# Kernel tuning notes

Measured on AMD Instinct MI355X. Metric: run time of the kernel, lower is better.

The kernel has to match this reference:

```python
import jax, jax.numpy as jnp
import numpy as np

N, F_IN, H, HEADS = 50000, 128, 128, 4
C = H // HEADS
E = 800000


def layer_norm(x, w, b, eps=1e-5):
    mu = x.mean(-1, keepdims=True)
    var = ((x - mu) ** 2).mean(-1, keepdims=True)
    return (x - mu) * jax.lax.rsqrt(var + eps) * w + b


def gat_conv(x, src, dst, edge_attr, W, att_src, att_dst, W_edge, att_edge, bias):
    """PyG GATConv (concat=True, add_self_loops=True, fill_value='mean', edge_dim=H), eval mode."""
    n = x.shape[0]
    # self-loop edge_attr = mean of incoming edge attrs per node (PyG fill_value='mean')
    ones = jnp.ones((src.shape[0],), dtype=edge_attr.dtype)
    deg = jax.ops.segment_sum(ones, dst, n)
    loop_attr = jax.ops.segment_sum(edge_attr, dst, n) / jnp.maximum(deg, 1.0)[:, None]
    loop = jnp.arange(n, dtype=src.dtype)
    src = jnp.concatenate([src, loop])
    dst = jnp.concatenate([dst, loop])
    ea = jnp.concatenate([edge_attr, loop_attr], axis=0)  # [E+N, H]
    h = (x @ W).reshape(n, HEADS, C)                      # [N, heads, C]
    a_src = (h * att_src).sum(-1)                         # [N, heads]
    a_dst = (h * att_dst).sum(-1)
    e = (ea @ W_edge).reshape(-1, HEADS, C)
    a_edge = (e * att_edge).sum(-1)                       # [E+N, heads]
    alpha = jax.nn.leaky_relu(a_src[src] + a_dst[dst] + a_edge, 0.2)
    # segment softmax over destination neighborhoods
    m = jax.lax.stop_gradient(jax.ops.segment_max(alpha, dst, n))
    alpha = jnp.exp(alpha - m[dst])
    s = jax.ops.segment_sum(alpha, dst, n)
    alpha = alpha / (s[dst] + 1e-16)
    out = jax.ops.segment_sum(alpha[:, :, None] * h[src], dst, n)  # [N, heads, C]
    return out.reshape(n, H) + bias


def setup_inputs() -> dict:
    key = jax.random.key(0)
    ks = iter(jax.random.split(key, 40))
    def lin(k, i, o, s=0.05):
        return jax.random.normal(k, (i, o), jnp.float32) * s
    d = {}
    d["x"] = jax.random.normal(next(ks), (N, F_IN), jnp.float32)
    d["edge_time"] = jax.random.uniform(next(ks), (E,), jnp.float32)
    d["ip_w1"] = lin(next(ks), F_IN, 2 * H); d["ip_b1"] = jnp.zeros((2 * H,), jnp.float32)
    d["ip_ln_w"] = jnp.ones((2 * H,), jnp.float32); d["ip_ln_b"] = jnp.zeros((2 * H,), jnp.float32)
    d["ip_w2"] = lin(next(ks), 2 * H, H); d["ip_b2"] = jnp.zeros((H,), jnp.float32)
    d["pn_w"] = jnp.ones((H,), jnp.float32); d["pn_b"] = jnp.zeros((H,), jnp.float32)
    d["ta_w1"] = lin(next(ks), 1, H); d["ta_b1"] = jnp.zeros((H,), jnp.float32)
    d["ta_ln_w"] = jnp.ones((H,), jnp.float32); d["ta_ln_b"] = jnp.zeros((H,), jnp.float32)
    d["ta_w2"] = lin(next(ks), H, H); d["ta_b2"] = jnp.zeros((H,), jnp.float32)
    for p in ("g1", "g2"):
        d[p + "_w"] = lin(next(ks), H, H)
        d[p + "_att_src"] = jax.random.normal(next(ks), (HEADS, C), jnp.float32) * 0.05
        d[p + "_att_dst"] = jax.random.normal(next(ks), (HEADS, C), jnp.float32) * 0.05
        d[p + "_ew"] = lin(next(ks), H, H)
        d[p + "_att_edge"] = jax.random.normal(next(ks), (HEADS, C), jnp.float32) * 0.05
        d[p + "_b"] = jnp.zeros((H,), jnp.float32)
    d["n1_w"] = jnp.ones((H,), jnp.float32); d["n1_b"] = jnp.zeros((H,), jnp.float32)
    d["n2_w"] = jnp.ones((H,), jnp.float32); d["n2_b"] = jnp.zeros((H,), jnp.float32)
    d["edge_index"] = jax.random.randint(next(ks), (2, E), 0, N, jnp.int32)
    return d


def reference(x, edge_time, ip_w1, ip_b1, ip_ln_w, ip_ln_b, ip_w2, ip_b2, pn_w, pn_b,
              ta_w1, ta_b1, ta_ln_w, ta_ln_b, ta_w2, ta_b2,
              g1_w, g1_att_src, g1_att_dst, g1_ew, g1_att_edge, g1_b,
              g2_w, g2_att_src, g2_att_dst, g2_ew, g2_att_edge, g2_b,
              n1_w, n1_b, n2_w, n2_b, edge_index):
    src, dst = edge_index[0], edge_index[1]
    # input projection: Linear -> ReLU -> LayerNorm -> (Dropout eval) -> Linear
    h = jax.nn.relu(x @ ip_w1 + ip_b1)
    h = layer_norm(h, ip_ln_w, ip_ln_b)
    h = h @ ip_w2 + ip_b2
    h = jnp.clip(jax.nn.relu(layer_norm(h, pn_w, pn_b)), -10.0, 10.0)
    # temporal attention MLP on edge times -> per-edge edge_attr [E, H]
    tw = edge_time[:, None] @ ta_w1 + ta_b1
    tw = jax.nn.relu(layer_norm(tw, ta_ln_w, ta_ln_b))
    tw = jnp.clip(jnp.tanh(tw @ ta_w2 + ta_b2), -3.0, 3.0)
    # GAT layer 1 (single chunk => residual + clamp, mean over 1 chunk is identity)
    g = gat_conv(h, src, dst, tw, g1_w, g1_att_src, g1_att_dst, g1_ew, g1_att_edge, g1_b) + h
    g = jax.nn.elu(layer_norm(jnp.clip(g, -10.0, 10.0), n1_w, n1_b))
    # GAT layer 2
    g2 = gat_conv(g, src, dst, tw, g2_w, g2_att_src, g2_att_dst, g2_ew, g2_att_edge, g2_b) + g
    return jax.nn.elu(layer_norm(jnp.clip(g2, -10.0, 10.0), n2_w, n2_b))
```

## Files before the change

kernel.cpp:

```cpp
#include <hip/hip_runtime.h>

typedef unsigned short u16;
typedef __attribute__((ext_vector_type(8))) short bf8_t;
typedef __attribute__((ext_vector_type(4))) float f4_t;

constexpr int NN   = 50000;
constexpr int NE   = 800000;
constexpr int TBLN = 2048;
constexpr int MB64 = (NN + 63) / 64;
constexpr int FB   = NE / 256;

__device__ __forceinline__ u16 f2b(float f) {
  unsigned u = __float_as_uint(f);
  unsigned r = u + 0x7fffu + ((u >> 16) & 1u);
  return (u16)(r >> 16);
}
__device__ __forceinline__ u16 f2h(float f) {
  _Float16 h = (_Float16)f;
  return __builtin_bit_cast(unsigned short, h);
}
__device__ __forceinline__ float h2f(u16 v) {
  _Float16 h = __builtin_bit_cast(_Float16, v);
  return (float)h;
}
__device__ __forceinline__ unsigned packh(float a, float b) {
  return (unsigned)f2h(a) | ((unsigned)f2h(b) << 16);
}
__device__ __forceinline__ float blo(unsigned u) { return __uint_as_float(u << 16); }
__device__ __forceinline__ float bhi(unsigned u) { return __uint_as_float(u & 0xffff0000u); }
__device__ __forceinline__ float wred64(float v) {
#pragma unroll
  for (int o = 32; o; o >>= 1) v += __shfl_xor(v, o);
  return v;
}
__device__ __forceinline__ bf8_t ldv(const u16* p) { return *(const bf8_t*)p; }
__device__ __forceinline__ f4_t mfma16(bf8_t a, bf8_t b, f4_t c) {
  return __builtin_amdgcn_mfma_f32_16x16x32_bf16(a, b, c, 0, 0, 0);
}

__global__ __launch_bounds__(256) void prep_k(
    const float* __restrict__ ew1, const float* __restrict__ ate1,
    const float* __restrict__ ew2, const float* __restrict__ ate2,
    float* __restrict__ V,
    const float* __restrict__ w1, const float* __restrict__ w2,
    const float* __restrict__ gw1, const float* __restrict__ gw2,
    u16* __restrict__ w1t, u16* __restrict__ w2t,
    u16* __restrict__ g1wt, u16* __restrict__ g2wt,
    const int* __restrict__ dstv, int* __restrict__ deg,
    const float* __restrict__ x, u16* __restrict__ x16) {
  const int bid = blockIdx.x, t = threadIdx.x;
  if (bid == 0) {
#pragma unroll
    for (int rep = 0; rep < 2; ++rep) {
      int idx = t + rep * 256;
      int k = idx >> 2, hd = idx & 3;
      float s1 = 0.f, s2 = 0.f;
      for (int c = 0; c < 32; ++c) {
        s1 += ew1[k * 128 + hd * 32 + c] * ate1[hd * 32 + c];
        s2 += ew2[k * 128 + hd * 32 + c] * ate2[hd * 32 + c];
      }
      V[k * 8 + hd] = s1;
      V[k * 8 + 4 + hd] = s2;
    }
  } else if (bid <= 384) {
    int idx = (bid - 1) * 256 + t;
    if (idx < 32768) {
      int r = idx >> 8, c = idx & 255;
      w1t[c * 128 + r] = f2b(w1[idx]);
    } else if (idx < 65536) {
      int k = idx - 32768;
      int r = k >> 7, c = k & 127;
      w2t[c * 256 + r] = f2b(w2[k]);
    } else if (idx < 81920) {
      int k = idx - 65536;
      int r = k >> 7, c = k & 127;
      g1wt[c * 128 + r] = f2b(gw1[k]);
    } else {
      int k = idx - 81920;
      int r = k >> 7, c = k & 127;
      g2wt[c * 128 + r] = f2b(gw2[k]);
    }
  } else if (bid <= 384 + FB) {
    int e = (bid - 385) * 256 + t;
    if (e < NE) atomicAdd(&deg[dstv[e]], 1);
  } else {
    int idx = (bid - 385 - FB) * 256 + t;
    size_t e8 = (size_t)idx * 8;
    const float4 a = *(const float4*)(x + e8);
    const float4 b = *(const float4*)(x + e8 + 4);
    uint4 o;
    o.x = (unsigned)f2b(a.x) | ((unsigned)f2b(a.y) << 16);
    o.y = (unsigned)f2b(a.z) | ((unsigned)f2b(a.w) << 16);
    o.z = (unsigned)f2b(b.x) | ((unsigned)f2b(b.y) << 16);
    o.w = (unsigned)f2b(b.z) | ((unsigned)f2b(b.w) << 16);
    *(uint4*)(x16 + e8) = o;
  }
}

__global__ __launch_bounds__(128) void build_table(
    const float* __restrict__ taw1, const float* __restrict__ tab1,
    const float* __restrict__ talnw, const float* __restrict__ talnb,
    const float* __restrict__ taw2, const float* __restrict__ tab2,
    const float* __restrict__ V, float* __restrict__ tbl) {
  const int j = threadIdx.x;
  const int wv = j >> 6, ln = j & 63;
  const float t = (float)blockIdx.x / (float)(TBLN - 1);
  __shared__ float part[4];
  __shared__ float ush[128];
  __shared__ float pacc[16];
  float v = t * taw1[j] + tab1[j];
  float s = wred64(v), sq = wred64(v * v);
  if (ln == 0) { part[wv * 2] = s; part[wv * 2 + 1] = sq; }
  __syncthreads();
  float S = part[0] + part[2], SQ = part[1] + part[3];
  float mu = S * (1.f / 128.f);
  float var = SQ * (1.f / 128.f) - mu * mu;
  float rstd = rsqrtf(var + 1e-5f);
  float u = fmaxf((v - mu) * rstd * talnw[j] + talnb[j], 0.f);
  ush[j] = u;
  __syncthreads();
  float acc = 0.f;
  for (int k = 0; k < 128; ++k) acc += ush[k] * taw2[k * 128 + j];
  float w = tanhf(acc + tab2[j]);
  w = fminf(fmaxf(w, -3.f), 3.f);
#pragma unroll
  for (int p = 0; p < 8; ++p) {
    float z = wred64(w * V[j * 8 + p]);
    if (ln == 0) pacc[wv * 8 + p] = z;
  }
  __syncthreads();
  if (j < 8) tbl[blockIdx.x * 8 + j] = pacc[j] + pacc[8 + j];
}

__global__ __launch_bounds__(512) void scan1(const int* __restrict__ deg,
                                             int* __restrict__ indptr,
                                             int* __restrict__ blks) {
  const int t = threadIdx.x;
  const int i = blockIdx.x * 512 + t;
  int v = (i < NN) ? deg[i] : 0;
  const int lane = t & 63, wv = t >> 6;
  int x = v;
#pragma unroll
  for (int o = 1; o < 64; o <<= 1) {
    int y = __shfl_up(x, o);
    if (lane >= o) x += y;
  }
  __shared__ int ws[8];
  if (lane == 63) ws[wv] = x;
  __syncthreads();
  if (t < 8) {
    int y = ws[t];
#pragma unroll
    for (int o = 1; o < 8; o <<= 1) {
      int z = __shfl_up(y, o);
      if (t >= o) y += z;
    }
    ws[t] = y;
  }
  __syncthreads();
  int excl = wv ? ws[wv - 1] : 0;
  x += excl;
  if (i < NN) indptr[i + 1] = x;
  if (t == 511) blks[blockIdx.x] = x;
}
__global__ void scan2(int* __restrict__ blks, int nb) {
  const int t = threadIdx.x;
  int v = (t < nb) ? blks[t] : 0;
  const int lane = t & 63, wv = t >> 6;
  int x = v;
#pragma unroll
  for (int o = 1; o < 64; o <<= 1) {
    int y = __shfl_up(x, o);
    if (lane >= o) x += y;
  }
  __shared__ int ws[2];
  if (lane == 63) ws[wv] = x;
  __syncthreads();
  if (wv == 1) x += ws[0];
  if (t < nb) blks[t] = x - v;
}
__global__ __launch_bounds__(512) void scan3(int* __restrict__ indptr,
                                             const int* __restrict__ blks,
                                             const int* __restrict__ deg,
                                             int* __restrict__ cursor) {
  const int i = blockIdx.x * 512 + threadIdx.x;
  if (i < NN) {
    int v = indptr[i + 1] + blks[blockIdx.x];
    indptr[i + 1] = v;
    cursor[i] = v - deg[i];
  }
  if (i == 0) indptr[0] = 0;
}

__device__ void fill_body(int fb, const int* __restrict__ srcv,
                          const int* __restrict__ dstv,
                          const float* __restrict__ etime,
                          const float* __restrict__ tbl,
                          int* __restrict__ cursor,
                          u16* __restrict__ recs) {
  const int e = fb * 256 + threadIdx.x;
  if (e >= NE) return;
  int d = dstv[e];
  int pos = atomicAdd(&cursor[d], 1);
  float t = etime[e];
  t = fminf(fmaxf(t, 0.f), 1.f);
  float fpos = t * (float)(TBLN - 1);
  int i0 = (int)fpos;
  if (i0 > TBLN - 2) i0 = TBLN - 2;
  float fr = fpos - (float)i0;
  const float4* r = (const float4*)(tbl + i0 * 8);
  float4 a0 = r[0], a1 = r[1], b0 = r[2], b1 = r[3];
  float4 o1, o2;
  o1.x = a0.x + fr * (b0.x - a0.x); o1.y = a0.y + fr * (b0.y - a0.y);
  o1.z = a0.z + fr * (b0.z - a0.z); o1.w = a0.w + fr * (b0.w - a0.w);
  o2.x = a1.x + fr * (b1.x - a1.x); o2.y = a1.y + fr * (b1.y - a1.y);
  o2.z = a1.z + fr * (b1.z - a1.z); o2.w = a1.w + fr * (b1.w - a1.w);
  u16* rp = recs + (size_t)pos * 16;
  uint4 w;
  w.x = (unsigned)srcv[e];
  w.y = packh(o1.x, o1.y);
  w.z = packh(o1.z, o1.w);
  w.w = packh(o2.x, o2.y);
  *(uint4*)rp = w;
  *(unsigned*)(rp + 8) = packh(o2.z, o2.w);
}

__device__ void ip_body(int ipb, char* smem,
                        const u16* __restrict__ x16, const u16* __restrict__ w1t,
                        const float* __restrict__ b1, const float* __restrict__ ln1w,
                        const float* __restrict__ ln1b, const u16* __restrict__ w2t,
                        const float* __restrict__ b2, const float* __restrict__ pnw,
                        const float* __restrict__ pnb, u16* __restrict__ h16,
                        const u16* __restrict__ g1wt, const float* __restrict__ attsrc,
                        const float* __restrict__ attdst, u16* __restrict__ hp16,
                        float* __restrict__ asrc, float* __restrict__ adst) {
  u16* h1n = (u16*)smem;
  u16* h2n = h1n;
  float* partS = (float*)(smem + 33792);
  float* partQ = (float*)(smem + 33792 + 1024);

  const int t = threadIdx.x;
  const int w = t >> 6, lane = t & 63, q = lane >> 4, l15 = lane & 15;
  const int rowbase = ipb * 64;

  f4_t acc[4][4];
#pragma unroll
  for (int mt = 0; mt < 4; ++mt)
#pragma unroll
    for (int nt = 0; nt < 4; ++nt) acc[mt][nt] = (f4_t){0.f, 0.f, 0.f, 0.f};
#pragma unroll
  for (int kst = 0; kst < 4; ++kst) {
    int k0 = kst * 32 + q * 8;
    bf8_t a[4];
#pragma unroll
    for (int mt = 0; mt < 4; ++mt) {
      int r = rowbase + mt * 16 + l15;
      if (r > NN - 1) r = NN - 1;
      a[mt] = ldv(x16 + (size_t)r * 128 + k0);
    }
#pragma unroll
    for (int nt = 0; nt < 4; ++nt) {
      int n = w * 64 + nt * 16 + l15;
      bf8_t b = ldv(w1t + n * 128 + k0);
#pragma unroll
      for (int mt = 0; mt < 4; ++mt)
        acc[mt][nt] = mfma16(a[mt], b, acc[mt][nt]);
    }
  }
#pragma unroll
  for (int nt = 0; nt < 4; ++nt) {
    float bb = b1[w * 64 + nt * 16 + l15];
#pragma unroll
    for (int mt = 0; mt < 4; ++mt)
#pragma unroll
      for (int r = 0; r < 4; ++r)
        acc[mt][nt][r] = fmaxf(acc[mt][nt][r] + bb, 0.f);
  }
  {
    float s[4][4], sq[4][4];
#pragma unroll
    for (int mt = 0; mt < 4; ++mt)
#pragma unroll
      for (int r = 0; r < 4; ++r) {
        float a0 = acc[mt][0][r], b0 = acc[mt][1][r], c0 = acc[mt][2][r], d0 = acc[mt][3][r];
        s[mt][r] = a0 + b0 + c0 + d0;
        sq[mt][r] = a0 * a0 + b0 * b0 + c0 * c0 + d0 * d0;
      }
#pragma unroll
    for (int o = 1; o < 16; o <<= 1)
#pragma unroll
      for (int mt = 0; mt < 4; ++mt)
#pragma unroll
        for (int r = 0; r < 4; ++r) {
          s[mt][r] += __shfl_xor(s[mt][r], o);
          sq[mt][r] += __shfl_xor(sq[mt][r], o);
        }
    if (l15 == 0) {
#pragma unroll
      for (int mt = 0; mt < 4; ++mt)
#pragma unroll
        for (int r = 0; r < 4; ++r) {
          int row = mt * 16 + q * 4 + r;
          partS[w * 64 + row] = s[mt][r];
          partQ[w * 64 + row] = sq[mt][r];
        }
    }
  }
  __syncthreads();
  {
    float lw[4], lb[4];
#pragma unroll
    for (int nt = 0; nt < 4; ++nt) {
      int col = w * 64 + nt * 16 + l15;
      lw[nt] = ln1w[col]; lb[nt] = ln1b[col];
    }
#pragma unroll
    for (int mt = 0; mt < 4; ++mt)
#pragma unroll
      for (int r = 0; r < 4; ++r) {
        int row = mt * 16 + q * 4 + r;
        float S = partS[row] + partS[64 + row] + partS[128 + row] + partS[192 + row];
        float Q = partQ[row] + partQ[64 + row] + partQ[128 + row] + partQ[192 + row];
        float mu = S * (1.f / 256.f);
        float var = Q * (1.f / 256.f) - mu * mu;
        float rstd = rsqrtf(var + 1e-5f);
#pragma unroll
        for (int nt = 0; nt < 4; ++nt) {
          int col = w * 64 + nt * 16 + l15;
          h1n[row * 264 + col] = f2b((acc[mt][nt][r] - mu) * rstd * lw[nt] + lb[nt]);
        }
      }
  }
  __syncthreads();
  f4_t acc2[4][2];
#pragma unroll
  for (int mt = 0; mt < 4; ++mt)
#pragma unroll
    for (int nt = 0; nt < 2; ++nt) acc2[mt][nt] = (f4_t){0.f, 0.f, 0.f, 0.f};
#pragma unroll
  for (int kst = 0; kst < 8; ++kst) {
    int k0 = kst * 32 + q * 8;
    bf8_t a[4];
#pragma unroll
    for (int mt = 0; mt < 4; ++mt)
      a[mt] = ldv(h1n + (mt * 16 + l15) * 264 + k0);
#pragma unroll
    for (int nt = 0; nt < 2; ++nt) {
      int n = w * 32 + nt * 16 + l15;
      bf8_t b = ldv(w2t + n * 256 + k0);
#pragma unroll
      for (int mt = 0; mt < 4; ++mt)
        acc2[mt][nt] = mfma16(a[mt], b, acc2[mt][nt]);
    }
  }
#pragma unroll
  for (int nt = 0; nt < 2; ++nt) {
    float bb = b2[w * 32 + nt * 16 + l15];
#pragma unroll
    for (int mt = 0; mt < 4; ++mt)
#pragma unroll
      for (int r = 0; r < 4; ++r)
        acc2[mt][nt][r] += bb;
  }
  {
    float s[4][4], sq[4][4];
#pragma unroll
    for (int mt = 0; mt < 4; ++mt)
#pragma unroll
      for (int r = 0; r < 4; ++r) {
        float a0 = acc2[mt][0][r], b0 = acc2[mt][1][r];
        s[mt][r] = a0 + b0;
        sq[mt][r] = a0 * a0 + b0 * b0;
      }
#pragma unroll
    for (int o = 1; o < 16; o <<= 1)
#pragma unroll
      for (int mt = 0; mt < 4; ++mt)
#pragma unroll
        for (int r = 0; r < 4; ++r) {
          s[mt][r] += __shfl_xor(s[mt][r], o);
          sq[mt][r] += __shfl_xor(sq[mt][r], o);
        }
    __syncthreads();
    if (l15 == 0) {
#pragma unroll
      for (int mt = 0; mt < 4; ++mt)
#pragma unroll
        for (int r = 0; r < 4; ++r) {
          int row = mt * 16 + q * 4 + r;
          partS[w * 64 + row] = s[mt][r];
          partQ[w * 64 + row] = sq[mt][r];
        }
    }
  }
  __syncthreads();
  {
    float lw[2], lb[2];
#pragma unroll
    for (int nt = 0; nt < 2; ++nt) {
      int col = w * 32 + nt * 16 + l15;
      lw[nt] = pnw[col]; lb[nt] = pnb[col];
    }
#pragma unroll
    for (int mt = 0; mt < 4; ++mt)
#pragma unroll
      for (int r = 0; r < 4; ++r) {
        int row = mt * 16 + q * 4 + r;
        float S = partS[row] + partS[64 + row] + partS[128 + row] + partS[192 + row];
        float Q = partQ[row] + partQ[64 + row] + partQ[128 + row] + partQ[192 + row];
        float mu = S * (1.f / 128.f);
        float var = Q * (1.f / 128.f) - mu * mu;
        float rstd = rsqrtf(var + 1e-5f);
#pragma unroll
        for (int nt = 0; nt < 2; ++nt) {
          int col = w * 32 + nt * 16 + l15;
          float v = (acc2[mt][nt][r] - mu) * rstd * lw[nt] + lb[nt];
          v = fminf(fmaxf(v, 0.f), 10.f);
          h2n[row * 136 + col] = f2b(v);
        }
      }
  }
  __syncthreads();
  {
    const int row = t >> 2, cb = (t & 3) * 32;
    int rg = rowbase + row;
    if (rg < NN) {
#pragma unroll
      for (int c = 0; c < 4; ++c) {
        uint4 v0 = *(const uint4*)(h2n + row * 136 + cb + c * 8);
        *(uint4*)(h16 + (size_t)rg * 128 + cb + c * 8) = v0;
      }
    }
  }
  f4_t acc3[4][2];
#pragma unroll
  for (int mt = 0; mt < 4; ++mt)
#pragma unroll
    for (int nt = 0; nt < 2; ++nt) acc3[mt][nt] = (f4_t){0.f, 0.f, 0.f, 0.f};
#pragma unroll
  for (int kst = 0; kst < 4; ++kst) {
    int k0 = kst * 32 + q * 8;
    bf8_t a[4];
#pragma unroll
    for (int mt = 0; mt < 4; ++mt)
      a[mt] = ldv(h2n + (mt * 16 + l15) * 136 + k0);
#pragma unroll
    for (int nt = 0; nt < 2; ++nt) {
      int n = w * 32 + nt * 16 + l15;
      bf8_t b = ldv(g1wt + n * 128 + k0);
#pragma unroll
      for (int mt = 0; mt < 4; ++mt)
        acc3[mt][nt] = mfma16(a[mt], b, acc3[mt][nt]);
    }
  }
  {
    float ps[4][4], pd[4][4];
#pragma unroll
    for (int mt = 0; mt < 4; ++mt)
#pragma unroll
      for (int r = 0; r < 4; ++r) { ps[mt][r] = 0.f; pd[mt][r] = 0.f; }
#pragma unroll
    for (int mt = 0; mt < 4; ++mt)
#pragma unroll
      for (int nt = 0; nt < 2; ++nt) {
        int col = w * 32 + nt * 16 + l15;
        float as = attsrc[col], ad = attdst[col];
#pragma unroll
        for (int r = 0; r < 4; ++r) {
          int row = mt * 16 + q * 4 + r;
          int rg = rowbase + row;
          float v = acc3[mt][nt][r];
          if (rg < NN) hp16[(size_t)rg * 128 + col] = f2b(v);
          ps[mt][r] += v * as;
          pd[mt][r] += v * ad;
        }
      }
#pragma unroll
    for (int o = 1; o < 16; o <<= 1)
#pragma unroll
      for (int mt = 0; mt < 4; ++mt)
#pragma unroll
        for (int r = 0; r < 4; ++r) {
          ps[mt][r] += __shfl_xor(ps[mt][r], o);
          pd[mt][r] += __shfl_xor(pd[mt][r], o);
        }
    if (l15 == 0) {
#pragma unroll
      for (int mt = 0; mt < 4; ++mt)
#pragma unroll
        for (int r = 0; r < 4; ++r) {
          int rg = rowbase + mt * 16 + q * 4 + r;
          if (rg < NN) {
            asrc[rg * 4 + w] = ps[mt][r];
            adst[rg * 4 + w] = pd[mt][r];
          }
        }
    }
  }
}

__global__ __launch_bounds__(256) void fillip_k(
    const int* srcv, const int* dstv, const float* etime, const float* tbl,
    int* cursor, u16* recs,
    const u16* x16, const u16* w1t, const float* b1, const float* ln1w,
    const float* ln1b, const u16* w2t, const float* b2, const float* pnw,
    const float* pnb, u16* h16,
    const u16* g1wt, const float* g1as, const float* g1ad,
    u16* hp16, float* asrc, float* adst) {
  __shared__ char smem[35840];
  const int bid = blockIdx.x;
  if (bid % 5 == 0) {
    ip_body(bid / 5, smem, x16, w1t, b1, ln1w, ln1b, w2t, b2, pnw, pnb, h16,
            g1wt, g1as, g1ad, hp16, asrc, adst);
  } else {
    fill_body(bid - bid / 5 - 1, srcv, dstv, etime, tbl, cursor, recs);
  }
}

__global__ __launch_bounds__(256) void hp_mfma(
    const u16* __restrict__ feat16, const u16* __restrict__ wt,
    const float* __restrict__ attsrc, const float* __restrict__ attdst,
    u16* __restrict__ hp16, float* __restrict__ asrc, float* __restrict__ adst) {
  const int t = threadIdx.x;
  const int w = t >> 6, lane = t & 63, q = lane >> 4, l15 = lane & 15;
  const int rowbase = blockIdx.x * 64;
  f4_t acc[4][2];
#pragma unroll
  for (int mt = 0; mt < 4; ++mt)
#pragma unroll
    for (int nt = 0; nt < 2; ++nt) acc[mt][nt] = (f4_t){0.f, 0.f, 0.f, 0.f};
#pragma unroll
  for (int kst = 0; kst < 4; ++kst) {
    int k0 = kst * 32 + q * 8;
    bf8_t a[4];
#pragma unroll
    for (int mt = 0; mt < 4; ++mt) {
      int r = rowbase + mt * 16 + l15;
      if (r > NN - 1) r = NN - 1;
      a[mt] = ldv(feat16 + (size_t)r * 128 + k0);
    }
#pragma unroll
    for (int nt = 0; nt < 2; ++nt) {
      int n = w * 32 + nt * 16 + l15;
      bf8_t b = ldv(wt + n * 128 + k0);
#pragma unroll
      for (int mt = 0; mt < 4; ++mt)
        acc[mt][nt] = mfma16(a[mt], b, acc[mt][nt]);
    }
  }
  float ps[4][4], pd[4][4];
#pragma unroll
  for (int mt = 0; mt < 4; ++mt)
#pragma unroll
    for (int r = 0; r < 4; ++r) { ps[mt][r] = 0.f; pd[mt][r] = 0.f; }
#pragma unroll
  for (int mt = 0; mt < 4; ++mt)
#pragma unroll
    for (int nt = 0; nt < 2; ++nt) {
      int col = w * 32 + nt * 16 + l15;
      float as = attsrc[col], ad = attdst[col];
#pragma unroll
      for (int r = 0; r < 4; ++r) {
        int row = mt * 16 + q * 4 + r;
        int rg = rowbase + row;
        float v = acc[mt][nt][r];
        if (rg < NN) hp16[(size_t)rg * 128 + col] = f2b(v);
        ps[mt][r] += v * as;
        pd[mt][r] += v * ad;
      }
    }
#pragma unroll
  for (int o = 1; o < 16; o <<= 1)
#pragma unroll
    for (int mt = 0; mt < 4; ++mt)
#pragma unroll
      for (int r = 0; r < 4; ++r) {
        ps[mt][r] += __shfl_xor(ps[mt][r], o);
        pd[mt][r] += __shfl_xor(pd[mt][r], o);
      }
  if (l15 == 0) {
#pragma unroll
    for (int mt = 0; mt < 4; ++mt)
#pragma unroll
      for (int r = 0; r < 4; ++r) {
        int rg = rowbase + mt * 16 + q * 4 + r;
        if (rg < NN) {
          asrc[rg * 4 + w] = ps[mt][r];
          adst[rg * 4 + w] = pd[mt][r];
        }
      }
  }
}

template <int L, int FINAL>
__global__ __launch_bounds__(256) void agg_k(
    const int* __restrict__ indptr, const u16* __restrict__ recs,
    const float* __restrict__ asrc, const float* __restrict__ adst,
    const u16* __restrict__ hp16, const u16* __restrict__ feat16,
    const float* __restrict__ gbias, const float* __restrict__ lnw,
    const float* __restrict__ lnb, u16* __restrict__ gout16,
    float* __restrict__ out32) {
  const int wv = threadIdx.x >> 6, lane = threadIdx.x & 63;
  const int n = blockIdx.x * 4 + wv;
  if (n >= NN) return;
  const int s0 = indptr[n], s1 = indptr[n + 1];
  const int dg = s1 - s0;
  const int g = lane >> 4, sl = lane & 15, cb = sl * 8, hdB = sl >> 2;
  const float advB = adst[n * 4 + hdB];
  float ssp = 0.f, sap = 0.f;
  float acc[8];
#pragma unroll
  for (int i = 0; i < 8; ++i) acc[i] = 0.f;
  for (int base = s0; base < s1; base += 8) {
    int i0 = base + g, i1 = base + 4 + g;
    int j0 = i0 < s1 ? i0 : s1 - 1;
    int j1 = i1 < s1 ? i1 : s1 - 1;
    const u16* r0 = recs + (size_t)j0 * 16;
    const u16* r1 = recs + (size_t)j1 * 16;
    int sc0 = *(const int*)r0, sc1 = *(const int*)r1;
    float ae0 = h2f(r0[2 + 4 * L + hdB]);
    float ae1v = h2f(r1[2 + 4 * L + hdB]);
    float as0 = asrc[sc0 * 4 + hdB], as1 = asrc[sc1 * 4 + hdB];
    const uint4 row0 = *(const uint4*)(hp16 + (size_t)sc0 * 128 + cb);
    const uint4 row1 = *(const uint4*)(hp16 + (size_t)sc1 * 128 + cb);
    float l0 = as0 + advB + ae0; l0 = fmaxf(l0, 0.2f * l0);
    float l1 = as1 + advB + ae1v; l1 = fmaxf(l1, 0.2f * l1);
    float w0 = (i0 < s1) ? __expf(l0) : 0.f;
    float w1 = (i1 < s1) ? __expf(l1) : 0.f;
    ssp += w0 + w1;
    sap += ((i0 < s1) ? ae0 : 0.f) + ((i1 < s1) ? ae1v : 0.f);
    acc[0] += w0 * blo(row0.x) + w1 * blo(row1.x);
    acc[1] += w0 * bhi(row0.x) + w1 * bhi(row1.x);
    acc[2] += w0 * blo(row0.y) + w1 * blo(row1.y);
    acc[3] += w0 * bhi(row0.y) + w1 * bhi(row1.y);
    acc[4] += w0 * blo(row0.z) + w1 * blo(row1.z);
    acc[5] += w0 * bhi(row0.z) + w1 * bhi(row1.z);
    acc[6] += w0 * blo(row0.w) + w1 * blo(row1.w);
    acc[7] += w0 * bhi(row0.w) + w1 * bhi(row1.w);
  }
#pragma unroll
  for (int i = 0; i < 8; ++i) {
    acc[i] += __shfl_xor(acc[i], 16);
    acc[i] += __shfl_xor(acc[i], 32);
  }
  ssp += __shfl_xor(ssp, 16); ssp += __shfl_xor(ssp, 32);
  sap += __shfl_xor(sap, 16); sap += __shfl_xor(sap, 32);
  const float degf = (float)(dg > 0 ? dg : 1);
  float asnB = asrc[n * 4 + hdB];
  float la = asnB + advB + sap / degf;
  la = fmaxf(la, 0.2f * la);
  float wsf = __expf(la);
  float inv = 1.f / (ssp + wsf + 1e-16f);
  const uint4 rs4 = *(const uint4*)(hp16 + (size_t)n * 128 + cb);
  const uint4 rr4 = *(const uint4*)(feat16 + (size_t)n * 128 + cb);
  const float4 gb0 = *(const float4*)(gbias + cb);
  const float4 gb1 = *(const float4*)(gbias + cb + 4);
  float v[8];
  v[0] = (acc[0] + wsf * blo(rs4.x)) * inv + gb0.x + blo(rr4.x);
  v[1] = (acc[1] + wsf * bhi(rs4.x)) * inv + gb0.y + bhi(rr4.x);
  v[2] = (acc[2] + wsf * blo(rs4.y)) * inv + gb0.z + blo(rr4.y);
  v[3] = (acc[3] + wsf * bhi(rs4.y)) * inv + gb0.w + bhi(rr4.y);
  v[4] = (acc[4] + wsf * blo(rs4.z)) * inv + gb1.x + blo(rr4.z);
  v[5] = (acc[5] + wsf * bhi(rs4.z)) * inv + gb1.y + bhi(rr4.z);
  v[6] = (acc[6] + wsf * blo(rs4.w)) * inv + gb1.z + blo(rr4.w);
  v[7] = (acc[7] + wsf * bhi(rs4.w)) * inv + gb1.w + bhi(rr4.w);
  float sum = 0.f, sq = 0.f;
#pragma unroll
  for (int i = 0; i < 8; ++i) {
    v[i] = fminf(fmaxf(v[i], -10.f), 10.f);
    sum += v[i]; sq += v[i] * v[i];
  }
#pragma unroll
  for (int o = 1; o < 16; o <<= 1) {
    sum += __shfl_xor(sum, o);
    sq += __shfl_xor(sq, o);
  }
  float mu = sum * (1.f / 128.f);
  float var = sq * (1.f / 128.f) - mu * mu;
  float rstd = rsqrtf(var + 1e-5f);
  const float4 lw0 = *(const float4*)(lnw + cb);
  const float4 lw1 = *(const float4*)(lnw + cb + 4);
  const float4 lb0 = *(const float4*)(lnb + cb);
  const float4 lb1 = *(const float4*)(lnb + cb + 4);
  float y[8];
  y[0] = (v[0] - mu) * rstd * lw0.x + lb0.x;
  y[1] = (v[1] - mu) * rstd * lw0.y + lb0.y;
  y[2] = (v[2] - mu) * rstd * lw0.z + lb0.z;
  y[3] = (v[3] - mu) * rstd * lw0.w + lb0.w;
  y[4] = (v[4] - mu) * rstd * lw1.x + lb1.x;
  y[5] = (v[5] - mu) * rstd * lw1.y + lb1.y;
  y[6] = (v[6] - mu) * rstd * lw1.z + lb1.z;
  y[7] = (v[7] - mu) * rstd * lw1.w + lb1.w;
#pragma unroll
  for (int i = 0; i < 8; ++i) y[i] = y[i] > 0.f ? y[i] : expm1f(y[i]);
  if (g == 0) {
    if (FINAL) {
      float4 o0 = {y[0], y[1], y[2], y[3]};
      float4 o1 = {y[4], y[5], y[6], y[7]};
      *(float4*)(out32 + (size_t)n * 128 + cb) = o0;
      *(float4*)(out32 + (size_t)n * 128 + cb + 4) = o1;
    } else {
      uint4 o;
      o.x = (unsigned)f2b(y[0]) | ((unsigned)f2b(y[1]) << 16);
      o.y = (unsigned)f2b(y[2]) | ((unsigned)f2b(y[3]) << 16);
      o.z = (unsigned)f2b(y[4]) | ((unsigned)f2b(y[5]) << 16);
      o.w = (unsigned)f2b(y[6]) | ((unsigned)f2b(y[7]) << 16);
      *(uint4*)(gout16 + (size_t)n * 128 + cb) = o;
    }
  }
}

extern "C" void kernel_launch(void* const* d_in, const int* in_sizes, int n_in,
                              void* d_out, int out_size, void* d_ws, size_t ws_size,
                              hipStream_t stream) {
  const float* x      = (const float*)d_in[0];
  const float* etime  = (const float*)d_in[1];
  const float* ip_w1  = (const float*)d_in[2];
  const float* ip_b1  = (const float*)d_in[3];
  const float* ip_lnw = (const float*)d_in[4];
  const float* ip_lnb = (const float*)d_in[5];
  const float* ip_w2  = (const float*)d_in[6];
  const float* ip_b2  = (const float*)d_in[7];
  const float* pn_w   = (const float*)d_in[8];
  const float* pn_b   = (const float*)d_in[9];
  const float* ta_w1  = (const float*)d_in[10];
  const float* ta_b1  = (const float*)d_in[11];
  const float* ta_lnw = (const float*)d_in[12];
  const float* ta_lnb = (const float*)d_in[13];
  const float* ta_w2  = (const float*)d_in[14];
  const float* ta_b2  = (const float*)d_in[15];
  const float* g1_w   = (const float*)d_in[16];
  const float* g1_as  = (const float*)d_in[17];
  const float* g1_ad  = (const float*)d_in[18];
  const float* g1_ew  = (const float*)d_in[19];
  const float* g1_ae  = (const float*)d_in[20];
  const float* g1_b   = (const float*)d_in[21];
  const float* g2_w   = (const float*)d_in[22];
  const float* g2_as  = (const float*)d_in[23];
  const float* g2_ad  = (const float*)d_in[24];
  const float* g2_ew  = (const float*)d_in[25];
  const float* g2_ae  = (const float*)d_in[26];
  const float* g2_b   = (const float*)d_in[27];
  const float* n1_w   = (const float*)d_in[28];
  const float* n1_b   = (const float*)d_in[29];
  const float* n2_w   = (const float*)d_in[30];
  const float* n2_b   = (const float*)d_in[31];
  const int* eidx     = (const int*)d_in[32];
  const int* srcv = eidx;
  const int* dstv = eidx + NE;

  char* p = (char*)d_ws;
  auto carve = [&](size_t bytes) -> char* {
    char* r = p;
    p += (bytes + 255) & ~(size_t)255;
    return r;
  };
  u16*   h16    = (u16*)carve((size_t)NN * 128 * 2);
  u16*   g16    = (u16*)carve((size_t)NN * 128 * 2);
  u16*   hp16   = (u16*)carve((size_t)NN * 128 * 2);
  float* asrc   = (float*)carve((size_t)NN * 4 * 4);
  float* adst   = (float*)carve((size_t)NN * 4 * 4);
  u16*   recs   = (u16*)carve((size_t)NE * 32);
  int*   deg    = (int*)carve((size_t)NN * 4);
  int*   indptr = (int*)carve((size_t)(NN + 1) * 4);
  int*   cursor = (int*)carve((size_t)NN * 4);
  int*   blks   = (int*)carve(512 * 4);
  float* V      = (float*)carve(128 * 8 * 4);
  float* tbl    = (float*)carve((size_t)TBLN * 8 * 4);
  u16*   w1t    = (u16*)carve(128 * 256 * 2);
  u16*   w2t    = (u16*)carve(256 * 128 * 2);
  u16*   g1wt   = (u16*)carve(128 * 128 * 2);
  u16*   g2wt   = (u16*)carve(128 * 128 * 2);
  u16*   x16    = (u16*)g16;

  hipMemsetAsync(deg, 0, (size_t)NN * 4, stream);

  const int SCB = (NN + 511) / 512;

  prep_k<<<1 + 384 + FB + FB, 256, 0, stream>>>(g1_ew, g1_ae, g2_ew, g2_ae, V,
                                                ip_w1, ip_w2, g1_w, g2_w,
                                                w1t, w2t, g1wt, g2wt, dstv, deg,
                                                x, x16);
  build_table<<<TBLN, 128, 0, stream>>>(ta_w1, ta_b1, ta_lnw, ta_lnb, ta_w2, ta_b2, V, tbl);
  scan1<<<SCB, 512, 0, stream>>>(deg, indptr, blks);
  scan2<<<1, 128, 0, stream>>>(blks, SCB);
  scan3<<<SCB, 512, 0, stream>>>(indptr, blks, deg, cursor);
  fillip_k<<<MB64 + FB, 256, 0, stream>>>(srcv, dstv, etime, tbl, cursor, recs,
                                          x16, w1t, ip_b1, ip_lnw, ip_lnb, w2t, ip_b2,
                                          pn_w, pn_b, h16,
                                          g1wt, g1_as, g1_ad, hp16, asrc, adst);
  agg_k<0, 0><<<NN / 4, 256, 0, stream>>>(indptr, recs, asrc, adst, hp16, h16,
                                          g1_b, n1_w, n1_b, g16, nullptr);
  hp_mfma<<<MB64, 256, 0, stream>>>(g16, g2wt, g2_as, g2_ad, hp16, asrc, adst);
  agg_k<1, 1><<<NN / 4, 256, 0, stream>>>(indptr, recs, asrc, adst, hp16, g16,
                                          g2_b, n2_w, n2_b, nullptr, (float*)d_out);
}
```

Before: 390.4 us.

## Fuse table build into prep kernel, merge scan stages, prefetch edge records

New measurement: 486.0 us. 24.5% more time.

```diff
diff --git a/kernel.cpp b/kernel.cpp
--- a/kernel.cpp
+++ b/kernel.cpp
@@ -9,6 +9,7 @@
 constexpr int TBLN = 2048;
 constexpr int MB64 = (NN + 63) / 64;
 constexpr int FB   = NE / 256;
+constexpr int TBB  = TBLN / 2;
 
 __device__ __forceinline__ u16 f2b(float f) {
   unsigned u = __float_as_uint(f);
@@ -33,6 +34,11 @@
   for (int o = 32; o; o >>= 1) v += __shfl_xor(v, o);
   return v;
 }
+__device__ __forceinline__ int iwred64(int v) {
+#pragma unroll
+  for (int o = 32; o; o >>= 1) v += __shfl_xor(v, o);
+  return v;
+}
 __device__ __forceinline__ bf8_t ldv(const u16* p) { return *(const bf8_t*)p; }
 __device__ __forceinline__ f4_t mfma16(bf8_t a, bf8_t b, f4_t c) {
   return __builtin_amdgcn_mfma_f32_16x16x32_bf16(a, b, c, 0, 0, 0);
@@ -41,29 +47,22 @@
 __global__ __launch_bounds__(256) void prep_k(
     const float* __restrict__ ew1, const float* __restrict__ ate1,
     const float* __restrict__ ew2, const float* __restrict__ ate2,
-    float* __restrict__ V,
     const float* __restrict__ w1, const float* __restrict__ w2,
     const float* __restrict__ gw1, const float* __restrict__ gw2,
     u16* __restrict__ w1t, u16* __restrict__ w2t,
     u16* __restrict__ g1wt, u16* __restrict__ g2wt,
     const int* __restrict__ dstv, int* __restrict__ deg,
-    const float* __restrict__ x, u16* __restrict__ x16) {
+    const float* __restrict__ x, u16* __restrict__ x16,
+    const float* __restrict__ taw1, const float* __restrict__ tab1,
+    const float* __restrict__ talnw, const float* __restrict__ talnb,
+    const float* __restrict__ taw2, const float* __restrict__ tab2,
+    float* __restrict__ tbl) {
+  __shared__ float tpart[2][4];
+  __shared__ float tush[2][128];
+  __shared__ float tpacc[2][16];
   const int bid = blockIdx.x, t = threadIdx.x;
-  if (bid == 0) {
-#pragma unroll
-    for (int rep = 0; rep < 2; ++rep) {
-      int idx = t + rep * 256;
-      int k = idx >> 2, hd = idx & 3;
-      float s1 = 0.f, s2 = 0.f;
-      for (int c = 0; c < 32; ++c) {
-        s1 += ew1[k * 128 + hd * 32 + c] * ate1[hd * 32 + c];
-        s2 += ew2[k * 128 + hd * 32 + c] * ate2[hd * 32 + c];
-      }
-      V[k * 8 + hd] = s1;
-      V[k * 8 + 4 + hd] = s2;
-    }
-  } else if (bid <= 384) {
-    int idx = (bid - 1) * 256 + t;
+  if (bid < 384) {
+    int idx = bid * 256 + t;
     if (idx < 32768) {
       int r = idx >> 8, c = idx & 255;
       w1t[c * 128 + r] = f2b(w1[idx]);
@@ -80,11 +79,11 @@
       int r = k >> 7, c = k & 127;
       g2wt[c * 128 + r] = f2b(gw2[k]);
     }
-  } else if (bid <= 384 + FB) {
-    int e = (bid - 385) * 256 + t;
+  } else if (bid < 384 + FB) {
+    int e = (bid - 384) * 256 + t;
     if (e < NE) atomicAdd(&deg[dstv[e]], 1);
-  } else {
-    int idx = (bid - 385 - FB) * 256 + t;
+  } else if (bid < 384 + 2 * FB) {
+    int idx = (bid - 384 - FB) * 256 + t;
     size_t e8 = (size_t)idx * 8;
     const float4 a = *(const float4*)(x + e8);
     const float4 b = *(const float4*)(x + e8 + 4);
@@ -94,42 +93,45 @@
     o.z = (unsigned)f2b(b.x) | ((unsigned)f2b(b.y) << 16);
     o.w = (unsigned)f2b(b.z) | ((unsigned)f2b(b.w) << 16);
     *(uint4*)(x16 + e8) = o;
-  }
-}
-
-__global__ __launch_bounds__(128) void build_table(
-    const float* __restrict__ taw1, const float* __restrict__ tab1,
-    const float* __restrict__ talnw, const float* __restrict__ talnb,
-    const float* __restrict__ taw2, const float* __restrict__ tab2,
-    const float* __restrict__ V, float* __restrict__ tbl) {
-  const int j = threadIdx.x;
-  const int wv = j >> 6, ln = j & 63;
-  const float t = (float)blockIdx.x / (float)(TBLN - 1);
-  __shared__ float part[4];
-  __shared__ float ush[128];
-  __shared__ float pacc[16];
-  float v = t * taw1[j] + tab1[j];
-  float s = wred64(v), sq = wred64(v * v);
-  if (ln == 0) { part[wv * 2] = s; part[wv * 2 + 1] = sq; }
-  __syncthreads();
-  float S = part[0] + part[2], SQ = part[1] + part[3];
-  float mu = S * (1.f / 128.f);
-  float var = SQ * (1.f / 128.f) - mu * mu;
-  float rstd = rsqrtf(var + 1e-5f);
-  float u = fmaxf((v - mu) * rstd * talnw[j] + talnb[j], 0.f);
-  ush[j] = u;
-  __syncthreads();
-  float acc = 0.f;
-  for (int k = 0; k < 128; ++k) acc += ush[k] * taw2[k * 128 + j];
-  float w = tanhf(acc + tab2[j]);
-  w = fminf(fmaxf(w, -3.f), 3.f);
-#pragma unroll
-  for (int p = 0; p < 8; ++p) {
-    float z = wred64(w * V[j * 8 + p]);
-    if (ln == 0) pacc[wv * 8 + p] = z;
-  }
-  __syncthreads();
-  if (j < 8) tbl[blockIdx.x * 8 + j] = pacc[j] + pacc[8 + j];
+  } else {
+    const int tb = bid - (384 + 2 * FB);
+    const int half = t >> 7, j = t & 127;
+    const int ln = t & 63, wvh = (t >> 6) & 1;
+    const float tv = (float)(tb * 2 + half) / (float)(TBLN - 1);
+    float Vloc[8];
+#pragma unroll
+    for (int p = 0; p < 4; ++p) {
+      float s1 = 0.f, s2 = 0.f;
+      for (int c = 0; c < 32; ++c) {
+        s1 += ew1[j * 128 + p * 32 + c] * ate1[p * 32 + c];
+        s2 += ew2[j * 128 + p * 32 + c] * ate2[p * 32 + c];
+      }
+      Vloc[p] = s1;
+      Vloc[4 + p] = s2;
+    }
+    float v = tv * taw1[j] + tab1[j];
+    float s = wred64(v), sq = wred64(v * v);
+    if (ln == 0) { tpart[half][wvh * 2] = s; tpart[half][wvh * 2 + 1] = sq; }
+    __syncthreads();
+    float S = tpart[half][0] + tpart[half][2], SQ = tpart[half][1] + tpart[half][3];
+    float mu = S * (1.f / 128.f);
+    float var = SQ * (1.f / 128.f) - mu * mu;
+    float rstd = rsqrtf(var + 1e-5f);
+    float u = fmaxf((v - mu) * rstd * talnw[j] + talnb[j], 0.f);
+    tush[half][j] = u;
+    __syncthreads();
+    float acc = 0.f;
+    for (int k = 0; k < 128; ++k) acc += tush[half][k] * taw2[k * 128 + j];
+    float w = tanhf(acc + tab2[j]);
+    w = fminf(fmaxf(w, -3.f), 3.f);
+#pragma unroll
+    for (int p = 0; p < 8; ++p) {
+      float z = wred64(w * Vloc[p]);
+      if (ln == 0) tpacc[half][wvh * 8 + p] = z;
+    }
+    __syncthreads();
+    if (j < 8) tbl[(tb * 2 + half) * 8 + j] = tpacc[half][j] + tpacc[half][8 + j];
+  }
 }
 
 __global__ __launch_bounds__(512) void scan1(const int* __restrict__ deg,
@@ -163,31 +165,23 @@
   if (i < NN) indptr[i + 1] = x;
   if (t == 511) blks[blockIdx.x] = x;
 }
-__global__ void scan2(int* __restrict__ blks, int nb) {
+__global__ __launch_bounds__(512) void scan23(int* __restrict__ indptr,
+                                              const int* __restrict__ blks,
+                                              const int* __restrict__ deg,
+                                              int* __restrict__ cursor, int nb) {
   const int t = threadIdx.x;
-  int v = (t < nb) ? blks[t] : 0;
-  const int lane = t & 63, wv = t >> 6;
-  int x = v;
-#pragma unroll
-  for (int o = 1; o < 64; o <<= 1) {
-    int y = __shfl_up(x, o);
-    if (lane >= o) x += y;
-  }
-  __shared__ int ws[2];
-  if (lane == 63) ws[wv] = x;
+  int v = (t < nb && t < blockIdx.x) ? blks[t] : 0;
+  const int wv = t >> 6;
+  int x = iwred64(v);
+  __shared__ int ws[8];
+  if ((t & 63) == 0) ws[wv] = x;
   __syncthreads();
-  if (wv == 1) x += ws[0];
-  if (t < nb) blks[t] = x - v;
-}
-__global__ __launch_bounds__(512) void scan3(int* __restrict__ indptr,
-                                             const int* __restrict__ blks,
-                                             const int* __restrict__ deg,
-                                             int* __restrict__ cursor) {
-  const int i = blockIdx.x * 512 + threadIdx.x;
+  int prefix = ws[0] + ws[1] + ws[2] + ws[3] + ws[4] + ws[5] + ws[6] + ws[7];
+  const int i = blockIdx.x * 512 + t;
   if (i < NN) {
-    int v = indptr[i + 1] + blks[blockIdx.x];
-    indptr[i + 1] = v;
-    cursor[i] = v - deg[i];
+    int val = indptr[i + 1] + prefix;
+    indptr[i + 1] = val;
+    cursor[i] = val - deg[i];
   }
   if (i == 0) indptr[0] = 0;
 }
@@ -611,15 +605,34 @@
   float acc[8];
 #pragma unroll
   for (int i = 0; i < 8; ++i) acc[i] = 0.f;
+  const int s1m1 = s1 - 1;
+  int pi0 = s0 + g, pi1 = s0 + 4 + g;
+  int pj0 = pi0 < s1 ? pi0 : s1m1, pj1 = pi1 < s1 ? pi1 : s1m1;
+  uint4 ra0 = *(const uint4*)(recs + (size_t)pj0 * 16);
+  unsigned rb0 = *(const unsigned*)(recs + (size_t)pj0 * 16 + 8);
+  uint4 ra1 = *(const uint4*)(recs + (size_t)pj1 * 16);
+  unsigned rb1 = *(const unsigned*)(recs + (size_t)pj1 * 16 + 8);
   for (int base = s0; base < s1; base += 8) {
+    uint4 nra0 = ra0, nra1 = ra1;
+    unsigned nrb0 = rb0, nrb1 = rb1;
+    int nbase = base + 8;
+    if (nbase < s1) {
+      int ni0 = nbase + g, ni1 = nbase + 4 + g;
+      int nj0 = ni0 < s1 ? ni0 : s1m1, nj1 = ni1 < s1 ? ni1 : s1m1;
+      nra0 = *(const uint4*)(recs + (size_t)nj0 * 16);
+      nrb0 = *(const unsigned*)(recs + (size_t)nj0 * 16 + 8);
+      nra1 = *(const uint4*)(recs + (size_t)nj1 * 16);
+      nrb1 = *(const unsigned*)(recs + (size_t)nj1 * 16 + 8);
+    }
     int i0 = base + g, i1 = base + 4 + g;
-    int j0 = i0 < s1 ? i0 : s1 - 1;
-    int j1 = i1 < s1 ? i1 : s1 - 1;
-    const u16* r0 = recs + (size_t)j0 * 16;
-    const u16* r1 = recs + (size_t)j1 * 16;
-    int sc0 = *(const int*)r0, sc1 = *(const int*)r1;
-    float ae0 = h2f(r0[2 + 4 * L + hdB]);
-    float ae1v = h2f(r1[2 + 4 * L + hdB]);
+    int sc0 = (int)ra0.x, sc1 = (int)ra1.x;
+    unsigned w00, w01, w10, w11;
+    if (L == 0) { w00 = ra0.y; w01 = ra0.z; w10 = ra1.y; w11 = ra1.z; }
+    else        { w00 = ra0.w; w01 = rb0;   w10 = ra1.w; w11 = rb1; }
+    unsigned sel0 = (hdB & 2) ? w01 : w00;
+    unsigned sel1 = (hdB & 2) ? w11 : w10;
+    float ae0 = h2f((u16)((hdB & 1) ? (sel0 >> 16) : (sel0 & 0xffffu)));
+    float ae1v = h2f((u16)((hdB & 1) ? (sel1 >> 16) : (sel1 & 0xffffu)));
     float as0 = asrc[sc0 * 4 + hdB], as1 = asrc[sc1 * 4 + hdB];
     const uint4 row0 = *(const uint4*)(hp16 + (size_t)sc0 * 128 + cb);
     const uint4 row1 = *(const uint4*)(hp16 + (size_t)sc1 * 128 + cb);
@@ -637,6 +650,7 @@
     acc[5] += w0 * bhi(row0.z) + w1 * bhi(row1.z);
     acc[6] += w0 * blo(row0.w) + w1 * blo(row1.w);
     acc[7] += w0 * bhi(row0.w) + w1 * bhi(row1.w);
+    ra0 = nra0; rb0 = nrb0; ra1 = nra1; rb1 = nrb1;
   }
 #pragma unroll
   for (int i = 0; i < 8; ++i) {
@@ -765,7 +779,6 @@
   int*   indptr = (int*)carve((size_t)(NN + 1) * 4);
   int*   cursor = (int*)carve((size_t)NN * 4);
   int*   blks   = (int*)carve(512 * 4);
-  float* V      = (float*)carve(128 * 8 * 4);
   float* tbl    = (float*)carve((size_t)TBLN * 8 * 4);
   u16*   w1t    = (u16*)carve(128 * 256 * 2);
   u16*   w2t    = (u16*)carve(256 * 128 * 2);
@@ -777,14 +790,14 @@
 
   const int SCB = (NN + 511) / 512;
 
-  prep_k<<<1 + 384 + FB + FB, 256, 0, stream>>>(g1_ew, g1_ae, g2_ew, g2_ae, V,
-                                                ip_w1, ip_w2, g1_w, g2_w,
-                                                w1t, w2t, g1wt, g2wt, dstv, deg,
-                                                x, x16);
-  build_table<<<TBLN, 128, 0, stream>>>(ta_w1, ta_b1, ta_lnw, ta_lnb, ta_w2, ta_b2, V, tbl);
+  prep_k<<<384 + 2 * FB + TBB, 256, 0, stream>>>(
+      g1_ew, g1_ae, g2_ew, g2_ae,
+      ip_w1, ip_w2, g1_w, g2_w,
+      w1t, w2t, g1wt, g2wt, dstv, deg,
+      x, x16,
+      ta_w1, ta_b1, ta_lnw, ta_lnb, ta_w2, ta_b2, tbl);
   scan1<<<SCB, 512, 0, stream>>>(deg, indptr, blks);
-  scan2<<<1, 128, 0, stream>>>(blks, SCB);
-  scan3<<<SCB, 512, 0, stream>>>(indptr, blks, deg, cursor);
+  scan23<<<SCB, 512, 0, stream>>>(indptr, blks, deg, cursor, SCB);
   fillip_k<<<MB64 + FB, 256, 0, stream>>>(srcv, dstv, etime, tbl, cursor, recs,
                                           x16, w1t, ip_b1, ip_lnw, ip_lnb, w2t, ip_b2,
                                           pn_w, pn_b, h16,
```
